# Performance work log

Hardware: AMD Instinct MI355X
Metric: run time of the kernel (lower is better)

The kernel has to match this reference:

```python
import jax, jax.numpy as jnp
import numpy as np


def _pairwise_sq_dists(t):
    # t: [B, L, R] -> [B, L, L] squared L2 distances via ||a||^2+||b||^2-2a.b
    sq = jnp.sum(t * t, axis=-1)                      # [B, L]
    dots = jnp.einsum('bir,bjr->bij', t, t)           # [B, L, L]
    d = sq[:, :, None] + sq[:, None, :] - 2.0 * dots
    return jnp.maximum(d, 0.0)


def setup_inputs() -> dict:
    key = jax.random.key(0)
    k1, k2, k3 = jax.random.split(key, 3)
    B, L, D, H, R = 16, 1024, 1024, 1024, 128
    batch = jax.random.normal(k1, (B, L, D), dtype=jnp.float32)
    # Linear weights stored as [in, out]; small init to keep activations sane
    W1 = jax.random.normal(k2, (D, H), dtype=jnp.float32) * (1.0 / np.sqrt(D))
    b1 = jnp.zeros((H,), dtype=jnp.float32)
    W2 = jax.random.normal(k3, (H, R), dtype=jnp.float32) * (1.0 / np.sqrt(H))
    b2 = jnp.zeros((R,), dtype=jnp.float32)
    return {"batch": batch, "W1": W1, "b1": b1, "W2": W2, "b2": b2}


def reference(batch, W1, b1, W2, b2):
    # layer 1: Linear + clamp(min=0)
    h = jnp.maximum(jnp.einsum('bld,dh->blh', batch, W1) + b1, 0.0)
    # layer 2 (projection to probe rank): Linear + clamp(min=0)
    t = jnp.maximum(jnp.einsum('blh,hr->blr', h, W2) + b2, 0.0)
    # all-pairs squared distances per sentence: [B, L, L]
    return _pairwise_sq_dists(t)
```

## Files before the change

kernel.cpp:

```cpp
#include <hip/hip_runtime.h>
#include <stdint.h>

#define B_ 16
#define L_ 1024
#define D_ 1024
#define H_ 1024
#define R_ 128
#define M_ (B_ * L_)

using f32x4  = __attribute__((ext_vector_type(4))) float;
using bf16x8 = __attribute__((ext_vector_type(8))) short;

__device__ __forceinline__ short f2bf(float f) {
  uint32_t u = __builtin_bit_cast(uint32_t, f);
  u = (u + 0x7FFFu + ((u >> 16) & 1u)) >> 16;
  return (short)(uint16_t)u;
}
__device__ __forceinline__ float bf2f(uint16_t h) {
  return __builtin_bit_cast(float, (uint32_t)h << 16);
}

__global__ void k_f32_to_bf16(const float* __restrict__ in, short* __restrict__ out) {
  size_t i = ((size_t)blockIdx.x * blockDim.x + threadIdx.x) * 8;
  float4 a = *(const float4*)(in + i);
  float4 b = *(const float4*)(in + i + 4);
  union { short s[8]; bf16x8 v; } o;
  o.s[0] = f2bf(a.x); o.s[1] = f2bf(a.y); o.s[2] = f2bf(a.z); o.s[3] = f2bf(a.w);
  o.s[4] = f2bf(b.x); o.s[5] = f2bf(b.y); o.s[6] = f2bf(b.z); o.s[7] = f2bf(b.w);
  *(bf16x8*)(out + i) = o.v;
}

__global__ void k_transpose_bf16(const float* __restrict__ in, short* __restrict__ out,
                                 int K, int N) {
  __shared__ float s[64][65];
  int n0 = blockIdx.x * 64, k0 = blockIdx.y * 64;
  int tx = threadIdx.x & 63, tq = threadIdx.x >> 6;
#pragma unroll
  for (int j = 0; j < 16; ++j) {
    int r = j * 4 + tq;
    s[r][tx] = in[(size_t)(k0 + r) * N + (n0 + tx)];
  }
  __syncthreads();
#pragma unroll
  for (int j = 0; j < 16; ++j) {
    int r = j * 4 + tq;
    out[(size_t)(n0 + r) * K + (k0 + tx)] = f2bf(s[tx][r]);
  }
}

__device__ __forceinline__ void gemm_body_128(const short* __restrict__ Ap,
                                              const short* __restrict__ Bp,
                                              int ld, int kSteps,
                                              short* As, short* Bs,
                                              f32x4 (&acc)[4][4]) {
  const int tid = threadIdx.x, lane = tid & 63, wave = tid >> 6;
  const int wr = wave >> 1, wc = wave & 1;
  const int lrow = lane & 15, lk8 = (lane >> 4) * 8;
  const int srow = lane >> 2;
  const int skc  = (lane & 3) * 8;

  for (int ks = 0; ks < kSteps; ++ks) {
    const int k0 = ks * 32;
#pragma unroll
    for (int c = 0; c < 2; ++c) {
      int chunk = wave * 2 + c;
      int row = chunk * 16 + srow;
      const short* ga = Ap + (size_t)row * ld + (k0 + skc);
      const short* gb = Bp + (size_t)row * ld + (k0 + skc);
      __builtin_amdgcn_global_load_lds(
          (const __attribute__((address_space(1))) void*)ga,
          (__attribute__((address_space(3))) void*)(As + chunk * 512 + lane * 8), 16, 0, 0);
      __builtin_amdgcn_global_load_lds(
          (const __attribute__((address_space(1))) void*)gb,
          (__attribute__((address_space(3))) void*)(Bs + chunk * 512 + lane * 8), 16, 0, 0);
    }
    __syncthreads();

    bf16x8 af[4], bfr[4];
#pragma unroll
    for (int m = 0; m < 4; ++m)
      af[m] = *(const bf16x8*)(As + (wr * 64 + m * 16 + lrow) * 32 + lk8);
#pragma unroll
    for (int n = 0; n < 4; ++n)
      bfr[n] = *(const bf16x8*)(Bs + (wc * 64 + n * 16 + lrow) * 32 + lk8);
#pragma unroll
    for (int m = 0; m < 4; ++m)
#pragma unroll
      for (int n = 0; n < 4; ++n)
        acc[m][n] = __builtin_amdgcn_mfma_f32_16x16x32_bf16(af[m], bfr[n], acc[m][n], 0, 0, 0);
    __syncthreads();
  }
}

__global__ __launch_bounds__(256)
void k_gemm1(const short* __restrict__ A, const short* __restrict__ Bt,
             const float* __restrict__ bias, short* __restrict__ C) {
  __shared__ __align__(16) short As[128 * 32];
  __shared__ __align__(16) short Bs[128 * 32];
  const int b = blockIdx.x;
  const int xcd = b & 7, seq = b >> 3;
  const int g = xcd + ((seq >> 6) << 3);
  const int i = seq & 63;
  const int m0 = (g * 8 + (i >> 3)) * 128;
  const int n0 = (i & 7) * 128;

  f32x4 acc[4][4] = {};
  gemm_body_128(A + (size_t)m0 * D_, Bt + (size_t)n0 * D_, D_, D_ / 32, As, Bs, acc);

  const int lane = threadIdx.x & 63, wave = threadIdx.x >> 6;
  const int wr = wave >> 1, wc = wave & 1;
  const int rbase = m0 + wr * 64 + (lane >> 4) * 4;
  const int cbase = n0 + wc * 64 + (lane & 15);
#pragma unroll
  for (int n = 0; n < 4; ++n) {
    const int col = cbase + n * 16;
    const float bn = bias[col];
#pragma unroll
    for (int m = 0; m < 4; ++m) {
      const int row = rbase + m * 16;
#pragma unroll
      for (int r = 0; r < 4; ++r) {
        float v = acc[m][n][r] + bn;
        C[(size_t)(row + r) * H_ + col] = f2bf(fmaxf(v, 0.f));
      }
    }
  }
}

__global__ __launch_bounds__(256)
void k_gemm2_splitk(const short* __restrict__ A, const short* __restrict__ Bt,
                    float* __restrict__ P) {
  __shared__ __align__(16) short As[128 * 32];
  __shared__ __align__(16) short Bs[128 * 32];
  const int m0 = blockIdx.y * 128;
  const int s  = blockIdx.z;
  const int kOff = s * (H_ / 4);

  f32x4 acc[4][4] = {};
  gemm_body_128(A + (size_t)m0 * H_ + kOff, Bt + kOff, H_, (H_ / 4) / 32, As, Bs, acc);

  const int lane = threadIdx.x & 63, wave = threadIdx.x >> 6;
  const int wr = wave >> 1, wc = wave & 1;
  const int rbase = wr * 64 + (lane >> 4) * 4;
  const int cbase = wc * 64 + (lane & 15);
  float* Ps = P + (size_t)s * M_ * R_ + (size_t)m0 * R_;
#pragma unroll
  for (int m = 0; m < 4; ++m)
#pragma unroll
    for (int r = 0; r < 4; ++r)
#pragma unroll
      for (int n = 0; n < 4; ++n)
        Ps[(size_t)(rbase + m * 16 + r) * R_ + cbase + n * 16] = acc[m][n][r];
}

__global__ void k_reduce2(const float* __restrict__ P, const float* __restrict__ b2,
                          short* __restrict__ T, float* __restrict__ sq) {
  const int row  = blockIdx.x * 4 + (threadIdx.x >> 6);
  const int lane = threadIdx.x & 63;
  const int c0 = lane * 2;
  float s0 = 0.f, s1 = 0.f;
#pragma unroll
  for (int s = 0; s < 4; ++s) {
    const float2 v = *(const float2*)(P + ((size_t)s * M_ + row) * R_ + c0);
    s0 += v.x; s1 += v.y;
  }
  float v0 = fmaxf(s0 + b2[c0], 0.f);
  float v1 = fmaxf(s1 + b2[c0 + 1], 0.f);
  uint32_t pk = (uint32_t)(uint16_t)f2bf(v0) | ((uint32_t)(uint16_t)f2bf(v1) << 16);
  *(uint32_t*)(T + (size_t)row * R_ + c0) = pk;
  float q = v0 * v0 + v1 * v1;
#pragma unroll
  for (int o = 32; o >= 1; o >>= 1) q += __shfl_xor(q, o, 64);
  if (lane == 0) sq[row] = q;
}

__global__ __launch_bounds__(256)
void k_pairwise(const short* __restrict__ T, const float* __restrict__ sq,
                float* __restrict__ out) {
  __shared__ __align__(16) short As[128 * 32];
  __shared__ __align__(16) short Bs[128 * 32];
  const int b = blockIdx.z;
  const short* Tb  = T  + (size_t)b * L_ * R_;
  const float* sqb = sq + (size_t)b * L_;
  const int m0 = blockIdx.y * 128, n0 = blockIdx.x * 128;

  f32x4 acc[4][4] = {};
  gemm_body_128(Tb + (size_t)m0 * R_, Tb + (size_t)n0 * R_, R_, R_ / 32, As, Bs, acc);

  const int lane = threadIdx.x & 63, wave = threadIdx.x >> 6;
  const int wr = wave >> 1, wc = wave & 1;
  const int rbase = m0 + wr * 64 + (lane >> 4) * 4;
  const int cbase = n0 + wc * 64 + (lane & 15);
  float sqj[4];
#pragma unroll
  for (int n = 0; n < 4; ++n) sqj[n] = sqb[cbase + n * 16];
#pragma unroll
  for (int m = 0; m < 4; ++m) {
#pragma unroll
    for (int r = 0; r < 4; ++r) {
      const int row = rbase + m * 16 + r;
      const float sqi = sqb[row];
      float* orow = out + ((size_t)b * L_ + row) * L_;
#pragma unroll
      for (int n = 0; n < 4; ++n) {
        float d = sqi + sqj[n] - 2.0f * acc[m][n][r];
        orow[cbase + n * 16] = fmaxf(d, 0.f);
      }
    }
  }
}

extern "C" void kernel_launch(void* const* d_in, const int* in_sizes, int n_in,
                              void* d_out, int out_size, void* d_ws, size_t ws_size,
                              hipStream_t stream) {
  const float* X  = (const float*)d_in[0];
  const float* W1 = (const float*)d_in[1];
  const float* b1 = (const float*)d_in[2];
  const float* W2 = (const float*)d_in[3];
  const float* b2 = (const float*)d_in[4];
  float* out = (float*)d_out;

  char* ws = (char*)d_ws;
  size_t off = 0;
  auto alloc = [&](size_t bytes) {
    char* p = ws + off;
    off += (bytes + 255) & ~(size_t)255;
    return p;
  };
  short* Xb  = (short*)alloc((size_t)M_ * D_ * 2);
  short* W1t = (short*)alloc((size_t)H_ * D_ * 2);
  short* Hb  = (short*)alloc((size_t)M_ * H_ * 2);
  short* W2t = (short*)alloc((size_t)R_ * H_ * 2);
  short* Tb  = (short*)alloc((size_t)M_ * R_ * 2);
  float* Sq  = (float*)alloc((size_t)M_ * 4);
  float* P   = (float*)Xb;

  k_f32_to_bf16<<<((size_t)M_ * D_) / 2048, 256, 0, stream>>>(X, Xb);
  k_transpose_bf16<<<dim3(H_ / 64, D_ / 64), 256, 0, stream>>>(W1, W1t, D_, H_);
  k_transpose_bf16<<<dim3(R_ / 64, H_ / 64), 256, 0, stream>>>(W2, W2t, H_, R_);
  k_gemm1<<<dim3((M_ / 128) * (H_ / 128)), 256, 0, stream>>>(Xb, W1t, b1, Hb);
  k_gemm2_splitk<<<dim3(1, M_ / 128, 4), 256, 0, stream>>>(Hb, W2t, P);
  k_reduce2<<<M_ / 4, 256, 0, stream>>>(P, b2, Tb, Sq);
  k_pairwise<<<dim3(L_ / 128, L_ / 128, B_), 256, 0, stream>>>(Tb, Sq, out);
}
```

Measured before the change: 209.6 us.

## Double-buffer LDS in GEMM bodies and merge prep kernels into one launch

The shared GEMM body now uses two LDS buffers, so the next K-slice's global-to-LDS loads are issued before computing on the current one. Explicit vmcnt waits, raw s_barrier, inline ds_read_b128 and setprio around the MFMA block replace the two full __syncthreads per step. The bf16 conversion and both weight transposes are merged into one k_prep launch to cut launch overhead. LDS use per block doubles, which may lower occupancy, and the hand-written waitcnt counts must stay correct for the load pattern.

```diff
diff --git a/kernel.cpp b/kernel.cpp
--- a/kernel.cpp
+++ b/kernel.cpp
@@ -20,21 +20,40 @@
   return __builtin_bit_cast(float, (uint32_t)h << 16);
 }
 
-__global__ void k_f32_to_bf16(const float* __restrict__ in, short* __restrict__ out) {
-  size_t i = ((size_t)blockIdx.x * blockDim.x + threadIdx.x) * 8;
-  float4 a = *(const float4*)(in + i);
-  float4 b = *(const float4*)(in + i + 4);
-  union { short s[8]; bf16x8 v; } o;
-  o.s[0] = f2bf(a.x); o.s[1] = f2bf(a.y); o.s[2] = f2bf(a.z); o.s[3] = f2bf(a.w);
-  o.s[4] = f2bf(b.x); o.s[5] = f2bf(b.y); o.s[6] = f2bf(b.z); o.s[7] = f2bf(b.w);
-  *(bf16x8*)(out + i) = o.v;
-}
-
-__global__ void k_transpose_bf16(const float* __restrict__ in, short* __restrict__ out,
-                                 int K, int N) {
+__device__ __forceinline__ bf16x8 lds_read_frag(const short* base, int elemOff) {
+  bf16x8 r;
+  const __attribute__((address_space(3))) short* p =
+      (const __attribute__((address_space(3))) short*)(base) + elemOff;
+  asm volatile("ds_read_b128 %0, %1" : "=v"(r) : "v"((uint32_t)(uintptr_t)p));
+  return r;
+}
+
+#define CONV_BLKS 8192
+#define T1B 256
+#define T2B 32
+__global__ void k_prep(const float* __restrict__ X, const float* __restrict__ W1,
+                       const float* __restrict__ W2, short* __restrict__ Xb,
+                       short* __restrict__ W1t, short* __restrict__ W2t) {
   __shared__ float s[64][65];
-  int n0 = blockIdx.x * 64, k0 = blockIdx.y * 64;
-  int tx = threadIdx.x & 63, tq = threadIdx.x >> 6;
+  const int b = blockIdx.x;
+  if (b < CONV_BLKS) {
+    size_t i = ((size_t)b * 256 + threadIdx.x) * 8;
+    float4 a = *(const float4*)(X + i);
+    float4 c = *(const float4*)(X + i + 4);
+    union { short sh[8]; bf16x8 v; } o;
+    o.sh[0] = f2bf(a.x); o.sh[1] = f2bf(a.y); o.sh[2] = f2bf(a.z); o.sh[3] = f2bf(a.w);
+    o.sh[4] = f2bf(c.x); o.sh[5] = f2bf(c.y); o.sh[6] = f2bf(c.z); o.sh[7] = f2bf(c.w);
+    *(bf16x8*)(Xb + i) = o.v;
+    return;
+  }
+  const float* in; short* out; int K, N, bx, by;
+  if (b < CONV_BLKS + T1B) {
+    int t = b - CONV_BLKS; in = W1; out = W1t; K = D_; N = H_; bx = t & 15; by = t >> 4;
+  } else {
+    int t = b - CONV_BLKS - T1B; in = W2; out = W2t; K = H_; N = R_; bx = t & 1; by = t >> 1;
+  }
+  const int n0 = bx * 64, k0 = by * 64;
+  const int tx = threadIdx.x & 63, tq = threadIdx.x >> 6;
 #pragma unroll
   for (int j = 0; j < 16; ++j) {
     int r = j * 4 + tq;
@@ -48,55 +67,70 @@
   }
 }
 
-__device__ __forceinline__ void gemm_body_128(const short* __restrict__ Ap,
-                                              const short* __restrict__ Bp,
-                                              int ld, int kSteps,
-                                              short* As, short* Bs,
-                                              f32x4 (&acc)[4][4]) {
+__device__ __forceinline__ void gemm_body_128_db(const short* __restrict__ Ap,
+                                                 const short* __restrict__ Bp,
+                                                 int ld, int kSteps,
+                                                 short* As, short* Bs,
+                                                 f32x4 (&acc)[4][4]) {
   const int tid = threadIdx.x, lane = tid & 63, wave = tid >> 6;
   const int wr = wave >> 1, wc = wave & 1;
   const int lrow = lane & 15, lk8 = (lane >> 4) * 8;
   const int srow = lane >> 2;
   const int skc  = (lane & 3) * 8;
 
+  auto STAGE = [&](int ks, int d) {
+    const int k0 = ks * 32;
+#pragma unroll
+    for (int c = 0; c < 2; ++c) {
+      const int chunk = wave * 2 + c;
+      const int row = chunk * 16 + srow;
+      __builtin_amdgcn_global_load_lds(
+          (const __attribute__((address_space(1))) void*)(Ap + (size_t)row * ld + (k0 + skc)),
+          (__attribute__((address_space(3))) void*)(As + d * 4096 + chunk * 512 + lane * 8), 16, 0, 0);
+      __builtin_amdgcn_global_load_lds(
+          (const __attribute__((address_space(1))) void*)(Bp + (size_t)row * ld + (k0 + skc)),
+          (__attribute__((address_space(3))) void*)(Bs + d * 4096 + chunk * 512 + lane * 8), 16, 0, 0);
+    }
+  };
+
+  STAGE(0, 0);
   for (int ks = 0; ks < kSteps; ++ks) {
-    const int k0 = ks * 32;
-#pragma unroll
-    for (int c = 0; c < 2; ++c) {
-      int chunk = wave * 2 + c;
-      int row = chunk * 16 + srow;
-      const short* ga = Ap + (size_t)row * ld + (k0 + skc);
-      const short* gb = Bp + (size_t)row * ld + (k0 + skc);
-      __builtin_amdgcn_global_load_lds(
-          (const __attribute__((address_space(1))) void*)ga,
-          (__attribute__((address_space(3))) void*)(As + chunk * 512 + lane * 8), 16, 0, 0);
-      __builtin_amdgcn_global_load_lds(
-          (const __attribute__((address_space(1))) void*)gb,
-          (__attribute__((address_space(3))) void*)(Bs + chunk * 512 + lane * 8), 16, 0, 0);
-    }
-    __syncthreads();
+    const int cur = ks & 1;
+    if (ks + 1 < kSteps) {
+      STAGE(ks + 1, cur ^ 1);
+      asm volatile("s_waitcnt vmcnt(4)" ::: "memory");
+    } else {
+      asm volatile("s_waitcnt vmcnt(0)" ::: "memory");
+    }
+    __builtin_amdgcn_s_barrier();
+    asm volatile("" ::: "memory");
 
     bf16x8 af[4], bfr[4];
 #pragma unroll
     for (int m = 0; m < 4; ++m)
-      af[m] = *(const bf16x8*)(As + (wr * 64 + m * 16 + lrow) * 32 + lk8);
+      af[m] = lds_read_frag(As, cur * 4096 + (wr * 64 + m * 16 + lrow) * 32 + lk8);
 #pragma unroll
     for (int n = 0; n < 4; ++n)
-      bfr[n] = *(const bf16x8*)(Bs + (wc * 64 + n * 16 + lrow) * 32 + lk8);
+      bfr[n] = lds_read_frag(Bs, cur * 4096 + (wc * 64 + n * 16 + lrow) * 32 + lk8);
+    asm volatile("s_waitcnt lgkmcnt(0)" ::: "memory");
+    __builtin_amdgcn_sched_barrier(0);
+    __builtin_amdgcn_s_setprio(1);
 #pragma unroll
     for (int m = 0; m < 4; ++m)
 #pragma unroll
       for (int n = 0; n < 4; ++n)
         acc[m][n] = __builtin_amdgcn_mfma_f32_16x16x32_bf16(af[m], bfr[n], acc[m][n], 0, 0, 0);
-    __syncthreads();
+    __builtin_amdgcn_s_setprio(0);
+    asm volatile("" ::: "memory");
+    __builtin_amdgcn_s_barrier();
   }
 }
 
 __global__ __launch_bounds__(256)
 void k_gemm1(const short* __restrict__ A, const short* __restrict__ Bt,
              const float* __restrict__ bias, short* __restrict__ C) {
-  __shared__ __align__(16) short As[128 * 32];
-  __shared__ __align__(16) short Bs[128 * 32];
+  __shared__ __align__(16) short As[2 * 4096];
+  __shared__ __align__(16) short Bs[2 * 4096];
   const int b = blockIdx.x;
   const int xcd = b & 7, seq = b >> 3;
   const int g = xcd + ((seq >> 6) << 3);
@@ -105,7 +139,7 @@
   const int n0 = (i & 7) * 128;
 
   f32x4 acc[4][4] = {};
-  gemm_body_128(A + (size_t)m0 * D_, Bt + (size_t)n0 * D_, D_, D_ / 32, As, Bs, acc);
+  gemm_body_128_db(A + (size_t)m0 * D_, Bt + (size_t)n0 * D_, D_, D_ / 32, As, Bs, acc);
 
   const int lane = threadIdx.x & 63, wave = threadIdx.x >> 6;
   const int wr = wave >> 1, wc = wave & 1;
@@ -130,14 +164,14 @@
 __global__ __launch_bounds__(256)
 void k_gemm2_splitk(const short* __restrict__ A, const short* __restrict__ Bt,
                     float* __restrict__ P) {
-  __shared__ __align__(16) short As[128 * 32];
-  __shared__ __align__(16) short Bs[128 * 32];
+  __shared__ __align__(16) short As[2 * 4096];
+  __shared__ __align__(16) short Bs[2 * 4096];
   const int m0 = blockIdx.y * 128;
   const int s  = blockIdx.z;
   const int kOff = s * (H_ / 4);
 
   f32x4 acc[4][4] = {};
-  gemm_body_128(A + (size_t)m0 * H_ + kOff, Bt + kOff, H_, (H_ / 4) / 32, As, Bs, acc);
+  gemm_body_128_db(A + (size_t)m0 * H_ + kOff, Bt + kOff, H_, (H_ / 4) / 32, As, Bs, acc);
 
   const int lane = threadIdx.x & 63, wave = threadIdx.x >> 6;
   const int wr = wave >> 1, wc = wave & 1;
@@ -177,15 +211,15 @@
 __global__ __launch_bounds__(256)
 void k_pairwise(const short* __restrict__ T, const float* __restrict__ sq,
                 float* __restrict__ out) {
-  __shared__ __align__(16) short As[128 * 32];
-  __shared__ __align__(16) short Bs[128 * 32];
+  __shared__ __align__(16) short As[2 * 4096];
+  __shared__ __align__(16) short Bs[2 * 4096];
   const int b = blockIdx.z;
   const short* Tb  = T  + (size_t)b * L_ * R_;
   const float* sqb = sq + (size_t)b * L_;
   const int m0 = blockIdx.y * 128, n0 = blockIdx.x * 128;
 
   f32x4 acc[4][4] = {};
-  gemm_body_128(Tb + (size_t)m0 * R_, Tb + (size_t)n0 * R_, R_, R_ / 32, As, Bs, acc);
+  gemm_body_128_db(Tb + (size_t)m0 * R_, Tb + (size_t)n0 * R_, R_, R_ / 32, As, Bs, acc);
 
   const int lane = threadIdx.x & 63, wave = threadIdx.x >> 6;
   const int wr = wave >> 1, wc = wave & 1;
@@ -235,9 +269,7 @@
   float* Sq  = (float*)alloc((size_t)M_ * 4);
   float* P   = (float*)Xb;
 
-  k_f32_to_bf16<<<((size_t)M_ * D_) / 2048, 256, 0, stream>>>(X, Xb);
-  k_transpose_bf16<<<dim3(H_ / 64, D_ / 64), 256, 0, stream>>>(W1, W1t, D_, H_);
-  k_transpose_bf16<<<dim3(R_ / 64, H_ / 64), 256, 0, stream>>>(W2, W2t, H_, R_);
+  k_prep<<<CONV_BLKS + T1B + T2B, 256, 0, stream>>>(X, W1, W2, Xb, W1t, W2t);
   k_gemm1<<<dim3((M_ / 128) * (H_ / 128)), 256, 0, stream>>>(Xb, W1t, b1, Hb);
   k_gemm2_splitk<<<dim3(1, M_ / 128, 4), 256, 0, stream>>>(Hb, W2t, P);
   k_reduce2<<<M_ / 4, 256, 0, stream>>>(P, b2, Tb, Sq);
```

Result: faster. 204.4 us (-2.5%).
